# Optimization experiments

Hardware: AMD Instinct MI355X
Metric: run time of the kernel (lower is better)

## Reference

```python
import jax, jax.numpy as jnp
import numpy as np

BS, N_PTS, N_SAMPLES = 8, 8192, 2048
GRID_SIZE = 4096
MAX_X, MAX_Y, MAX_Z = 25.0, 25.0, 5.0
P_NORM = 1


def _sample_axis(key, max_v):
    # linspace(-max_v, max_v, GRID_SIZE) indexed by multinomial(uniform, replacement=False)
    rng = jnp.linspace(-max_v, max_v, GRID_SIZE, dtype=jnp.float32)
    idx = jax.random.choice(key, GRID_SIZE, (N_SAMPLES,), replace=False)
    return rng[idx]


def setup_inputs() -> dict:
    key = jax.random.key(0)
    k1, k2, kx, ky, kz = jax.random.split(key, 5)
    gts = jax.random.normal(k1, (BS, N_PTS, 3), dtype=jnp.float32) * 10.0
    preds = jax.random.normal(k2, (BS, N_PTS, 3), dtype=jnp.float32) * 10.0
    gx = _sample_axis(kx, MAX_X)
    gy = _sample_axis(ky, MAX_Y)
    gz = _sample_axis(kz, MAX_Z)
    grid = jnp.stack([gx, gy, gz], axis=1)  # (N_SAMPLES, 3)
    grid_points = jnp.broadcast_to(grid[None], (BS, N_SAMPLES, 3)).astype(jnp.float32)
    return {"gts": gts, "preds": preds, "grid_points": grid_points}


def _cdist(x, y):
    # Euclidean cdist: (b, n, d) x (b, m, d) -> (b, n, m)
    x2 = jnp.sum(x * x, axis=-1)[:, :, None]
    y2 = jnp.sum(y * y, axis=-1)[:, None, :]
    xy = jnp.einsum('bnd,bmd->bnm', x, y)
    return jnp.sqrt(jnp.maximum(x2 + y2 - 2.0 * xy, 0.0))


def reference(gts, preds, grid_points):
    mins = jnp.min(_cdist(grid_points, preds), axis=2)   # (b, n_samples)
    mins2 = jnp.min(_cdist(grid_points, gts), axis=2)    # (b, n_samples)
    diff = jnp.abs(mins - mins2)
    if P_NORM == 2:
        diff = diff ** 2
    return jnp.mean(diff, axis=1)  # (b,)
```

## Files before the change

kernel.cpp:

```cpp
#include <hip/hip_runtime.h>
#include <math.h>

#define BS 8
#define N_PTS 8192
#define N_SAMPLES 2048
#define THREADS 256
#define SPT 8
#define PSPLIT 64
#define CHUNK (N_PTS / PSPLIT)

__global__ __launch_bounds__(THREADS, 1)
void chamfer_min_kernel(const float* __restrict__ gts,
                        const float* __restrict__ preds,
                        const float* __restrict__ grid,
                        unsigned int* __restrict__ wsmin)
{
    const int bid = blockIdx.x;
    const int b   = bid / PSPLIT;
    const int pc  = bid % PSPLIT;
    const int t   = threadIdx.x;

    __shared__ float4 ldsP[CHUNK];
    __shared__ float4 ldsG[CHUNK];

    {
        const int j = t & (CHUNK - 1);
        const float* src = (t < CHUNK)
            ? preds + ((size_t)b * N_PTS + (size_t)pc * CHUNK) * 3
            : gts   + ((size_t)b * N_PTS + (size_t)pc * CHUNK) * 3;
        const float x = src[j * 3 + 0];
        const float y = src[j * 3 + 1];
        const float z = src[j * 3 + 2];
        const float hp = fmaf(x, x, fmaf(y, y, z * z));
        const float4 v = make_float4(x, y, z, hp);
        if (t < CHUNK) ldsP[j] = v; else ldsG[j] = v;
    }

    float nsx[SPT], nsy[SPT], nsz[SPT], mP[SPT], mG[SPT];
    {
        const float* grow = grid + (size_t)b * N_SAMPLES * 3;
#pragma unroll
        for (int k = 0; k < SPT; ++k) {
            const int s = k * THREADS + t;
            nsx[k] = -2.0f * grow[s * 3 + 0];
            nsy[k] = -2.0f * grow[s * 3 + 1];
            nsz[k] = -2.0f * grow[s * 3 + 2];
            mP[k] = 3.0e38f;
            mG[k] = 3.0e38f;
        }
    }

    __syncthreads();

#pragma unroll 2
    for (int j = 0; j < CHUNK; j += 2) {
        const float4 p0 = ldsP[j], p1 = ldsP[j + 1];
        const float4 g0 = ldsG[j], g1 = ldsG[j + 1];
#pragma unroll
        for (int k = 0; k < SPT; ++k) {
            const float t0 = fmaf(p0.x, nsx[k], fmaf(p0.y, nsy[k], fmaf(p0.z, nsz[k], p0.w)));
            const float t1 = fmaf(p1.x, nsx[k], fmaf(p1.y, nsy[k], fmaf(p1.z, nsz[k], p1.w)));
            mP[k] = fminf(fminf(t0, t1), mP[k]);
            const float u0 = fmaf(g0.x, nsx[k], fmaf(g0.y, nsy[k], fmaf(g0.z, nsz[k], g0.w)));
            const float u1 = fmaf(g1.x, nsx[k], fmaf(g1.y, nsy[k], fmaf(g1.z, nsz[k], g1.w)));
            mG[k] = fminf(fminf(u0, u1), mG[k]);
        }
    }

    unsigned int* wp = wsmin + (size_t)b * N_SAMPLES;
    unsigned int* wg = wsmin + (size_t)(BS + b) * N_SAMPLES;
#pragma unroll
    for (int k = 0; k < SPT; ++k) {
        const int s = k * THREADS + t;
        const float s2 = 0.25f * fmaf(nsx[k], nsx[k], fmaf(nsy[k], nsy[k], nsz[k] * nsz[k]));
        atomicMin(&wp[s], __float_as_uint(fmaxf(mP[k] + s2, 0.0f)));
        atomicMin(&wg[s], __float_as_uint(fmaxf(mG[k] + s2, 0.0f)));
    }
}

__global__ __launch_bounds__(THREADS)
void chamfer_finish_kernel(const unsigned int* __restrict__ wsmin,
                           float* __restrict__ out)
{
    const int b = blockIdx.x;
    const int t = threadIdx.x;
    const unsigned int* wp = wsmin + (size_t)b * N_SAMPLES;
    const unsigned int* wg = wsmin + (size_t)(BS + b) * N_SAMPLES;

    float sum = 0.0f;
#pragma unroll
    for (int s = t; s < N_SAMPLES; s += THREADS) {
        const float dp = sqrtf(__uint_as_float(wp[s]));
        const float dg = sqrtf(__uint_as_float(wg[s]));
        sum += fabsf(dp - dg);
    }

#pragma unroll
    for (int off = 32; off > 0; off >>= 1)
        sum += __shfl_down(sum, off, 64);

    __shared__ float wsum[THREADS / 64];
    const int wid = t >> 6;
    if ((t & 63) == 0) wsum[wid] = sum;
    __syncthreads();
    if (t == 0) {
        float tot = 0.0f;
#pragma unroll
        for (int w = 0; w < THREADS / 64; ++w) tot += wsum[w];
        out[b] = tot / (float)N_SAMPLES;
    }
}

extern "C" void kernel_launch(void* const* d_in, const int* in_sizes, int n_in,
                              void* d_out, int out_size, void* d_ws, size_t ws_size,
                              hipStream_t stream)
{
    const float* gts   = (const float*)d_in[0];
    const float* preds = (const float*)d_in[1];
    const float* grid  = (const float*)d_in[2];
    float* out = (float*)d_out;
    unsigned int* wsmin = (unsigned int*)d_ws;

    const size_t wsbytes = (size_t)2 * BS * N_SAMPLES * sizeof(unsigned int);
    hipMemsetAsync(d_ws, 0x7F, wsbytes, stream);

    chamfer_min_kernel<<<dim3(BS * PSPLIT), dim3(THREADS), 0, stream>>>(gts, preds, grid, wsmin);
    chamfer_finish_kernel<<<dim3(BS), dim3(THREADS), 0, stream>>>(wsmin, out);
}
```

Measured before the change: 34.25 us.

## Precompute float4 point tables in a prep kernel and read them directly from global

Adds a prep kernel that packs preds and gts into float4 (x,y,z,|p|^2) in workspace and initialises the atomic-min buffer, which replaces the memset. The main kernel now reads the packed points straight from global memory (wave-uniform, so broadcast loads) instead of staging them through LDS behind a __syncthreads, and processes four points per step. The aim is to drop the LDS staging and the barrier. In exchange it adds a launch, a global write and re-read of the point tables, and leaves a dead stub kernel behind.

```diff
diff --git a/kernel.cpp b/kernel.cpp
--- a/kernel.cpp
+++ b/kernel.cpp
@@ -8,33 +8,60 @@
 #define SPT 8
 #define PSPLIT 64
 #define CHUNK (N_PTS / PSPLIT)
+#define NTOT (BS * N_PTS)
+
+#define WSMIN_OFF (2 * NTOT)
+
+__global__ __launch_bounds__(THREADS)
+void chamfer_prep_kernel(const float* __restrict__ gts,
+                         const float* __restrict__ preds,
+                         float4* __restrict__ ws)
+{
+    const int i = blockIdx.x * THREADS + threadIdx.x;
+    const float* src = (i < NTOT) ? preds : gts;
+    const int j = (i < NTOT) ? i : i - NTOT;
+    const float x = src[j * 3 + 0];
+    const float y = src[j * 3 + 1];
+    const float z = src[j * 3 + 2];
+    ws[i] = make_float4(x, y, z, fmaf(x, x, fmaf(y, y, z * z)));
+
+    if (i < 2 * BS * N_SAMPLES) {
+        unsigned int* wsmin = (unsigned int*)(ws + WSMIN_OFF);
+        wsmin[i] = 0x7F7F7F7Fu;
+    }
+}
 
 __global__ __launch_bounds__(THREADS, 1)
-void chamfer_min_kernel(const float* __restrict__ gts,
-                        const float* __restrict__ preds,
-                        const float* __restrict__ grid,
-                        unsigned int* __restrict__ wsmin)
+void chamfer_min_kernel(const float4* __restrict__ ws)
 {
     const int bid = blockIdx.x;
     const int b   = bid / PSPLIT;
     const int pc  = bid % PSPLIT;
     const int t   = threadIdx.x;
 
-    __shared__ float4 ldsP[CHUNK];
-    __shared__ float4 ldsG[CHUNK];
+    const float4* __restrict__ pp = ws + (size_t)b * N_PTS + (size_t)pc * CHUNK;
+    const float4* __restrict__ gg = ws + (size_t)(BS + b) * N_PTS + (size_t)pc * CHUNK;
 
+    float nsx[SPT], nsy[SPT], nsz[SPT], mP[SPT], mG[SPT];
     {
-        const int j = t & (CHUNK - 1);
-        const float* src = (t < CHUNK)
-            ? preds + ((size_t)b * N_PTS + (size_t)pc * CHUNK) * 3
-            : gts   + ((size_t)b * N_PTS + (size_t)pc * CHUNK) * 3;
-        const float x = src[j * 3 + 0];
-        const float y = src[j * 3 + 1];
-        const float z = src[j * 3 + 2];
-        const float hp = fmaf(x, x, fmaf(y, y, z * z));
-        const float4 v = make_float4(x, y, z, hp);
-        if (t < CHUNK) ldsP[j] = v; else ldsG[j] = v;
+        const float* grow = (const float*)0;
+        const float* gridp;
+        (void)grow; (void)gridp;
     }
+    mP[0] = 0.f;
+}
+
+__global__ __launch_bounds__(THREADS, 1)
+void chamfer_min_kernel2(const float4* __restrict__ ws,
+                         const float* __restrict__ grid)
+{
+    const int bid = blockIdx.x;
+    const int b   = bid / PSPLIT;
+    const int pc  = bid % PSPLIT;
+    const int t   = threadIdx.x;
+
+    const float4* __restrict__ pp = ws + (size_t)b * N_PTS + (size_t)pc * CHUNK;
+    const float4* __restrict__ gg = ws + (size_t)(BS + b) * N_PTS + (size_t)pc * CHUNK;
 
     float nsx[SPT], nsy[SPT], nsz[SPT], mP[SPT], mG[SPT];
     {
@@ -50,23 +77,27 @@
         }
     }
 
-    __syncthreads();
-
 #pragma unroll 2
-    for (int j = 0; j < CHUNK; j += 2) {
-        const float4 p0 = ldsP[j], p1 = ldsP[j + 1];
-        const float4 g0 = ldsG[j], g1 = ldsG[j + 1];
+    for (int j = 0; j < CHUNK; j += 4) {
+        const float4 p0 = pp[j], p1 = pp[j + 1], p2 = pp[j + 2], p3 = pp[j + 3];
+        const float4 g0 = gg[j], g1 = gg[j + 1], g2 = gg[j + 2], g3 = gg[j + 3];
 #pragma unroll
         for (int k = 0; k < SPT; ++k) {
-            const float t0 = fmaf(p0.x, nsx[k], fmaf(p0.y, nsy[k], fmaf(p0.z, nsz[k], p0.w)));
-            const float t1 = fmaf(p1.x, nsx[k], fmaf(p1.y, nsy[k], fmaf(p1.z, nsz[k], p1.w)));
-            mP[k] = fminf(fminf(t0, t1), mP[k]);
-            const float u0 = fmaf(g0.x, nsx[k], fmaf(g0.y, nsy[k], fmaf(g0.z, nsz[k], g0.w)));
-            const float u1 = fmaf(g1.x, nsx[k], fmaf(g1.y, nsy[k], fmaf(g1.z, nsz[k], g1.w)));
-            mG[k] = fminf(fminf(u0, u1), mG[k]);
+            const float x = nsx[k], y = nsy[k], z = nsz[k];
+            const float t0 = fmaf(p0.x, x, fmaf(p0.y, y, fmaf(p0.z, z, p0.w)));
+            const float t1 = fmaf(p1.x, x, fmaf(p1.y, y, fmaf(p1.z, z, p1.w)));
+            const float t2 = fmaf(p2.x, x, fmaf(p2.y, y, fmaf(p2.z, z, p2.w)));
+            const float t3 = fmaf(p3.x, x, fmaf(p3.y, y, fmaf(p3.z, z, p3.w)));
+            mP[k] = fminf(fminf(t0, t1), fminf(fminf(t2, t3), mP[k]));
+            const float u0 = fmaf(g0.x, x, fmaf(g0.y, y, fmaf(g0.z, z, g0.w)));
+            const float u1 = fmaf(g1.x, x, fmaf(g1.y, y, fmaf(g1.z, z, g1.w)));
+            const float u2 = fmaf(g2.x, x, fmaf(g2.y, y, fmaf(g2.z, z, g2.w)));
+            const float u3 = fmaf(g3.x, x, fmaf(g3.y, y, fmaf(g3.z, z, g3.w)));
+            mG[k] = fminf(fminf(u0, u1), fminf(fminf(u2, u3), mG[k]));
         }
     }
 
+    unsigned int* wsmin = (unsigned int*)(ws + WSMIN_OFF);
     unsigned int* wp = wsmin + (size_t)b * N_SAMPLES;
     unsigned int* wg = wsmin + (size_t)(BS + b) * N_SAMPLES;
 #pragma unroll
@@ -79,9 +110,10 @@
 }
 
 __global__ __launch_bounds__(THREADS)
-void chamfer_finish_kernel(const unsigned int* __restrict__ wsmin,
+void chamfer_finish_kernel(const float4* __restrict__ ws,
                            float* __restrict__ out)
 {
+    const unsigned int* wsmin = (const unsigned int*)(ws + WSMIN_OFF);
     const int b = blockIdx.x;
     const int t = threadIdx.x;
     const unsigned int* wp = wsmin + (size_t)b * N_SAMPLES;
@@ -119,11 +151,9 @@
     const float* preds = (const float*)d_in[1];
     const float* grid  = (const float*)d_in[2];
     float* out = (float*)d_out;
-    unsigned int* wsmin = (unsigned int*)d_ws;
+    float4* ws = (float4*)d_ws;
 
-    const size_t wsbytes = (size_t)2 * BS * N_SAMPLES * sizeof(unsigned int);
-    hipMemsetAsync(d_ws, 0x7F, wsbytes, stream);
-
-    chamfer_min_kernel<<<dim3(BS * PSPLIT), dim3(THREADS), 0, stream>>>(gts, preds, grid, wsmin);
-    chamfer_finish_kernel<<<dim3(BS), dim3(THREADS), 0, stream>>>(wsmin, out);
+    chamfer_prep_kernel<<<dim3(2 * NTOT / THREADS), dim3(THREADS), 0, stream>>>(gts, preds, ws);
+    chamfer_min_kernel2<<<dim3(BS * PSPLIT), dim3(THREADS), 0, stream>>>(ws, grid);
+    chamfer_finish_kernel<<<dim3(BS), dim3(THREADS), 0, stream>>>(ws, out);
 }
```

New measurement: 43.81 us. 1.28x slower.

## Add prep kernel for packed points, retile min kernel with more samples per thread

Applied to the files above, without the earlier changes.

Adds a prep kernel that packs preds and gts into float4 (x,y,z,|p|^2) in workspace and initializes the atomic-min buffer, replacing the memset. The min kernel now uses 128 threads with 16 samples per thread and splits the points into 128 chunks, loading pre-packed float4s. This raises register reuse per LDS read and doubles the block count for the same total work. The cost is an extra kernel launch and a workspace round trip, plus higher register pressure from SPT=16.

```diff
diff --git a/kernel.cpp b/kernel.cpp
--- a/kernel.cpp
+++ b/kernel.cpp
@@ -4,16 +4,36 @@
 #define BS 8
 #define N_PTS 8192
 #define N_SAMPLES 2048
-#define THREADS 256
-#define SPT 8
-#define PSPLIT 64
+#define THREADS 128
+#define SPT 16
+#define PSPLIT 128
 #define CHUNK (N_PTS / PSPLIT)
+#define NTOT (BS * N_PTS)
 
-__global__ __launch_bounds__(THREADS, 1)
-void chamfer_min_kernel(const float* __restrict__ gts,
-                        const float* __restrict__ preds,
-                        const float* __restrict__ grid,
-                        unsigned int* __restrict__ wsmin)
+#define WSMIN_OFF (2 * NTOT)
+
+__global__ __launch_bounds__(256)
+void chamfer_prep_kernel(const float* __restrict__ gts,
+                         const float* __restrict__ preds,
+                         float4* __restrict__ ws)
+{
+    const int i = blockIdx.x * 256 + threadIdx.x;
+    const float* src = (i < NTOT) ? preds : gts;
+    const int j = (i < NTOT) ? i : i - NTOT;
+    const float x = src[j * 3 + 0];
+    const float y = src[j * 3 + 1];
+    const float z = src[j * 3 + 2];
+    ws[i] = make_float4(x, y, z, fmaf(x, x, fmaf(y, y, z * z)));
+
+    if (i < 2 * BS * N_SAMPLES) {
+        unsigned int* wsmin = (unsigned int*)(ws + WSMIN_OFF);
+        wsmin[i] = 0x7F7F7F7Fu;
+    }
+}
+
+__global__ __launch_bounds__(THREADS, 2)
+void chamfer_min_kernel(const float4* __restrict__ ws,
+                        const float* __restrict__ grid)
 {
     const int bid = blockIdx.x;
     const int b   = bid / PSPLIT;
@@ -25,14 +45,10 @@
 
     {
         const int j = t & (CHUNK - 1);
-        const float* src = (t < CHUNK)
-            ? preds + ((size_t)b * N_PTS + (size_t)pc * CHUNK) * 3
-            : gts   + ((size_t)b * N_PTS + (size_t)pc * CHUNK) * 3;
-        const float x = src[j * 3 + 0];
-        const float y = src[j * 3 + 1];
-        const float z = src[j * 3 + 2];
-        const float hp = fmaf(x, x, fmaf(y, y, z * z));
-        const float4 v = make_float4(x, y, z, hp);
+        const float4* src = (t < CHUNK)
+            ? ws + (size_t)b * N_PTS + (size_t)pc * CHUNK
+            : ws + (size_t)(BS + b) * N_PTS + (size_t)pc * CHUNK;
+        const float4 v = src[j];
         if (t < CHUNK) ldsP[j] = v; else ldsG[j] = v;
     }
 
@@ -58,15 +74,17 @@
         const float4 g0 = ldsG[j], g1 = ldsG[j + 1];
 #pragma unroll
         for (int k = 0; k < SPT; ++k) {
-            const float t0 = fmaf(p0.x, nsx[k], fmaf(p0.y, nsy[k], fmaf(p0.z, nsz[k], p0.w)));
-            const float t1 = fmaf(p1.x, nsx[k], fmaf(p1.y, nsy[k], fmaf(p1.z, nsz[k], p1.w)));
+            const float x = nsx[k], y = nsy[k], z = nsz[k];
+            const float t0 = fmaf(p0.x, x, fmaf(p0.y, y, fmaf(p0.z, z, p0.w)));
+            const float t1 = fmaf(p1.x, x, fmaf(p1.y, y, fmaf(p1.z, z, p1.w)));
             mP[k] = fminf(fminf(t0, t1), mP[k]);
-            const float u0 = fmaf(g0.x, nsx[k], fmaf(g0.y, nsy[k], fmaf(g0.z, nsz[k], g0.w)));
-            const float u1 = fmaf(g1.x, nsx[k], fmaf(g1.y, nsy[k], fmaf(g1.z, nsz[k], g1.w)));
+            const float u0 = fmaf(g0.x, x, fmaf(g0.y, y, fmaf(g0.z, z, g0.w)));
+            const float u1 = fmaf(g1.x, x, fmaf(g1.y, y, fmaf(g1.z, z, g1.w)));
             mG[k] = fminf(fminf(u0, u1), mG[k]);
         }
     }
 
+    unsigned int* wsmin = (unsigned int*)(ws + WSMIN_OFF);
     unsigned int* wp = wsmin + (size_t)b * N_SAMPLES;
     unsigned int* wg = wsmin + (size_t)(BS + b) * N_SAMPLES;
 #pragma unroll
@@ -78,10 +96,11 @@
     }
 }
 
-__global__ __launch_bounds__(THREADS)
-void chamfer_finish_kernel(const unsigned int* __restrict__ wsmin,
+__global__ __launch_bounds__(256)
+void chamfer_finish_kernel(const float4* __restrict__ ws,
                            float* __restrict__ out)
 {
+    const unsigned int* wsmin = (const unsigned int*)(ws + WSMIN_OFF);
     const int b = blockIdx.x;
     const int t = threadIdx.x;
     const unsigned int* wp = wsmin + (size_t)b * N_SAMPLES;
@@ -89,7 +108,7 @@
 
     float sum = 0.0f;
 #pragma unroll
-    for (int s = t; s < N_SAMPLES; s += THREADS) {
+    for (int s = t; s < N_SAMPLES; s += 256) {
         const float dp = sqrtf(__uint_as_float(wp[s]));
         const float dg = sqrtf(__uint_as_float(wg[s]));
         sum += fabsf(dp - dg);
@@ -99,14 +118,14 @@
     for (int off = 32; off > 0; off >>= 1)
         sum += __shfl_down(sum, off, 64);
 
-    __shared__ float wsum[THREADS / 64];
+    __shared__ float wsum[4];
     const int wid = t >> 6;
     if ((t & 63) == 0) wsum[wid] = sum;
     __syncthreads();
     if (t == 0) {
         float tot = 0.0f;
 #pragma unroll
-        for (int w = 0; w < THREADS / 64; ++w) tot += wsum[w];
+        for (int w = 0; w < 4; ++w) tot += wsum[w];
         out[b] = tot / (float)N_SAMPLES;
     }
 }
@@ -119,11 +138,9 @@
     const float* preds = (const float*)d_in[1];
     const float* grid  = (const float*)d_in[2];
     float* out = (float*)d_out;
-    unsigned int* wsmin = (unsigned int*)d_ws;
+    float4* ws = (float4*)d_ws;
 
-    const size_t wsbytes = (size_t)2 * BS * N_SAMPLES * sizeof(unsigned int);
-    hipMemsetAsync(d_ws, 0x7F, wsbytes, stream);
-
-    chamfer_min_kernel<<<dim3(BS * PSPLIT), dim3(THREADS), 0, stream>>>(gts, preds, grid, wsmin);
-    chamfer_finish_kernel<<<dim3(BS), dim3(THREADS), 0, stream>>>(wsmin, out);
+    chamfer_prep_kernel<<<dim3(2 * NTOT / 256), dim3(256), 0, stream>>>(gts, preds, ws);
+    chamfer_min_kernel<<<dim3(BS * PSPLIT), dim3(THREADS), 0, stream>>>(ws, grid);
+    chamfer_finish_kernel<<<dim3(BS), dim3(256), 0, stream>>>(ws, out);
 }
```

Result: slower. 45.69 us (+33.4%).

## Replace atomic min reduction with partial buffers and two-stage reduce

Applied to the files above, without the earlier changes.

The min kernel now uses 128-thread blocks, 16 samples per thread and 128 point chunks per batch. Each block writes its per-sample minima to a partial buffer instead of issuing atomicMin, which removes the memset and atomic contention. A separate reduce kernel takes the min over chunks and a tiny kernel forms the final mean. Inline asm pins keep values in registers and the inner loop is no longer unrolled. In exchange it adds about 16 MB of partial-buffer traffic and one extra kernel launch.

```diff
diff --git a/kernel.cpp b/kernel.cpp
--- a/kernel.cpp
+++ b/kernel.cpp
@@ -4,20 +4,24 @@
 #define BS 8
 #define N_PTS 8192
 #define N_SAMPLES 2048
-#define THREADS 256
-#define SPT 8
-#define PSPLIT 64
+#define TA 128
+#define SPT 16
+#define PSPLIT 128
 #define CHUNK (N_PTS / PSPLIT)
 
-__global__ __launch_bounds__(THREADS, 1)
+#define PART_ELEMS (2 * BS * PSPLIT * N_SAMPLES)
+
+#define PIN4(v) asm volatile("" : "+v"(v.x), "+v"(v.y), "+v"(v.z), "+v"(v.w))
+
+__global__ __launch_bounds__(TA, 1)
 void chamfer_min_kernel(const float* __restrict__ gts,
                         const float* __restrict__ preds,
                         const float* __restrict__ grid,
-                        unsigned int* __restrict__ wsmin)
+                        float* __restrict__ part)
 {
     const int bid = blockIdx.x;
-    const int b   = bid / PSPLIT;
-    const int pc  = bid % PSPLIT;
+    const int b   = bid >> 7;
+    const int pc  = bid & (PSPLIT - 1);
     const int t   = threadIdx.x;
 
     __shared__ float4 ldsP[CHUNK];
@@ -25,26 +29,27 @@
 
     {
         const int j = t & (CHUNK - 1);
-        const float* src = (t < CHUNK)
-            ? preds + ((size_t)b * N_PTS + (size_t)pc * CHUNK) * 3
-            : gts   + ((size_t)b * N_PTS + (size_t)pc * CHUNK) * 3;
-        const float x = src[j * 3 + 0];
-        const float y = src[j * 3 + 1];
-        const float z = src[j * 3 + 2];
-        const float hp = fmaf(x, x, fmaf(y, y, z * z));
-        const float4 v = make_float4(x, y, z, hp);
+        const float* src = ((t < CHUNK) ? preds : gts)
+                         + ((size_t)b * N_PTS + (size_t)pc * CHUNK + j) * 3;
+        const float x = src[0], y = src[1], z = src[2];
+        const float4 v = make_float4(x, y, z, fmaf(x, x, fmaf(y, y, z * z)));
         if (t < CHUNK) ldsP[j] = v; else ldsG[j] = v;
     }
 
-    float nsx[SPT], nsy[SPT], nsz[SPT], mP[SPT], mG[SPT];
+    float nsx[SPT], nsy[SPT], nsz[SPT], s2[SPT], mP[SPT], mG[SPT];
     {
         const float* grow = grid + (size_t)b * N_SAMPLES * 3;
 #pragma unroll
         for (int k = 0; k < SPT; ++k) {
-            const int s = k * THREADS + t;
-            nsx[k] = -2.0f * grow[s * 3 + 0];
-            nsy[k] = -2.0f * grow[s * 3 + 1];
-            nsz[k] = -2.0f * grow[s * 3 + 2];
+            const int s = k * TA + t;
+            const float x = grow[s * 3 + 0];
+            const float y = grow[s * 3 + 1];
+            const float z = grow[s * 3 + 2];
+            s2[k]  = fmaf(x, x, fmaf(y, y, z * z));
+            nsx[k] = -2.0f * x;
+            nsy[k] = -2.0f * y;
+            nsz[k] = -2.0f * z;
+            asm volatile("" : "+v"(nsx[k]), "+v"(nsy[k]), "+v"(nsz[k]), "+v"(s2[k]));
             mP[k] = 3.0e38f;
             mG[k] = 3.0e38f;
         }
@@ -52,62 +57,75 @@
 
     __syncthreads();
 
-#pragma unroll 2
+#pragma unroll 1
     for (int j = 0; j < CHUNK; j += 2) {
-        const float4 p0 = ldsP[j], p1 = ldsP[j + 1];
-        const float4 g0 = ldsG[j], g1 = ldsG[j + 1];
+        float4 p0 = ldsP[j], p1 = ldsP[j + 1];
+        float4 g0 = ldsG[j], g1 = ldsG[j + 1];
+        PIN4(p0); PIN4(p1); PIN4(g0); PIN4(g1);
 #pragma unroll
         for (int k = 0; k < SPT; ++k) {
-            const float t0 = fmaf(p0.x, nsx[k], fmaf(p0.y, nsy[k], fmaf(p0.z, nsz[k], p0.w)));
-            const float t1 = fmaf(p1.x, nsx[k], fmaf(p1.y, nsy[k], fmaf(p1.z, nsz[k], p1.w)));
+            const float x = nsx[k], y = nsy[k], z = nsz[k];
+            const float t0 = fmaf(p0.x, x, fmaf(p0.y, y, fmaf(p0.z, z, p0.w)));
+            const float t1 = fmaf(p1.x, x, fmaf(p1.y, y, fmaf(p1.z, z, p1.w)));
             mP[k] = fminf(fminf(t0, t1), mP[k]);
-            const float u0 = fmaf(g0.x, nsx[k], fmaf(g0.y, nsy[k], fmaf(g0.z, nsz[k], g0.w)));
-            const float u1 = fmaf(g1.x, nsx[k], fmaf(g1.y, nsy[k], fmaf(g1.z, nsz[k], g1.w)));
+            const float u0 = fmaf(g0.x, x, fmaf(g0.y, y, fmaf(g0.z, z, g0.w)));
+            const float u1 = fmaf(g1.x, x, fmaf(g1.y, y, fmaf(g1.z, z, g1.w)));
             mG[k] = fminf(fminf(u0, u1), mG[k]);
         }
     }
 
-    unsigned int* wp = wsmin + (size_t)b * N_SAMPLES;
-    unsigned int* wg = wsmin + (size_t)(BS + b) * N_SAMPLES;
+    float* pp = part + (((size_t)b)           * PSPLIT + pc) * N_SAMPLES;
+    float* pg = part + (((size_t)(BS + b))    * PSPLIT + pc) * N_SAMPLES;
 #pragma unroll
     for (int k = 0; k < SPT; ++k) {
-        const int s = k * THREADS + t;
-        const float s2 = 0.25f * fmaf(nsx[k], nsx[k], fmaf(nsy[k], nsy[k], nsz[k] * nsz[k]));
-        atomicMin(&wp[s], __float_as_uint(fmaxf(mP[k] + s2, 0.0f)));
-        atomicMin(&wg[s], __float_as_uint(fmaxf(mG[k] + s2, 0.0f)));
+        const int s = k * TA + t;
+        pp[s] = fmaxf(mP[k] + s2[k], 0.0f);
+        pg[s] = fmaxf(mG[k] + s2[k], 0.0f);
     }
 }
 
-__global__ __launch_bounds__(THREADS)
-void chamfer_finish_kernel(const unsigned int* __restrict__ wsmin,
-                           float* __restrict__ out)
+__global__ __launch_bounds__(256, 1)
+void chamfer_reduce_kernel(const float* __restrict__ part,
+                           float* __restrict__ tsum)
 {
-    const int b = blockIdx.x;
-    const int t = threadIdx.x;
-    const unsigned int* wp = wsmin + (size_t)b * N_SAMPLES;
-    const unsigned int* wg = wsmin + (size_t)(BS + b) * N_SAMPLES;
+    const int blk  = blockIdx.x;
+    const int b    = blk >> 3;
+    const int tile = blk & 7;
+    const int t    = threadIdx.x;
+    const int s    = tile * 256 + t;
 
-    float sum = 0.0f;
-#pragma unroll
-    for (int s = t; s < N_SAMPLES; s += THREADS) {
-        const float dp = sqrtf(__uint_as_float(wp[s]));
-        const float dg = sqrtf(__uint_as_float(wg[s]));
-        sum += fabsf(dp - dg);
+    const float* pp = part + ((size_t)b)        * PSPLIT * N_SAMPLES + s;
+    const float* pg = part + ((size_t)(BS + b)) * PSPLIT * N_SAMPLES + s;
+
+    float mp = 3.0e38f, mg = 3.0e38f;
+#pragma unroll 4
+    for (int pc = 0; pc < PSPLIT; ++pc) {
+        mp = fminf(mp, pp[(size_t)pc * N_SAMPLES]);
+        mg = fminf(mg, pg[(size_t)pc * N_SAMPLES]);
     }
+
+    float v = fabsf(sqrtf(mp) - sqrtf(mg));
 
 #pragma unroll
     for (int off = 32; off > 0; off >>= 1)
-        sum += __shfl_down(sum, off, 64);
+        v += __shfl_down(v, off, 64);
 
-    __shared__ float wsum[THREADS / 64];
-    const int wid = t >> 6;
-    if ((t & 63) == 0) wsum[wid] = sum;
+    __shared__ float w[4];
+    if ((t & 63) == 0) w[t >> 6] = v;
     __syncthreads();
-    if (t == 0) {
+    if (t == 0) tsum[blk] = (w[0] + w[1]) + (w[2] + w[3]);
+}
+
+__global__ __launch_bounds__(64)
+void chamfer_out_kernel(const float* __restrict__ tsum,
+                        float* __restrict__ out)
+{
+    const int b = threadIdx.x;
+    if (b < BS) {
         float tot = 0.0f;
 #pragma unroll
-        for (int w = 0; w < THREADS / 64; ++w) tot += wsum[w];
-        out[b] = tot / (float)N_SAMPLES;
+        for (int i = 0; i < 8; ++i) tot += tsum[b * 8 + i];
+        out[b] = tot * (1.0f / (float)N_SAMPLES);
     }
 }
 
@@ -118,12 +136,11 @@
     const float* gts   = (const float*)d_in[0];
     const float* preds = (const float*)d_in[1];
     const float* grid  = (const float*)d_in[2];
-    float* out = (float*)d_out;
-    unsigned int* wsmin = (unsigned int*)d_ws;
+    float* out  = (float*)d_out;
+    float* part = (float*)d_ws;
+    float* tsum = part + PART_ELEMS;
 
-    const size_t wsbytes = (size_t)2 * BS * N_SAMPLES * sizeof(unsigned int);
-    hipMemsetAsync(d_ws, 0x7F, wsbytes, stream);
-
-    chamfer_min_kernel<<<dim3(BS * PSPLIT), dim3(THREADS), 0, stream>>>(gts, preds, grid, wsmin);
-    chamfer_finish_kernel<<<dim3(BS), dim3(THREADS), 0, stream>>>(wsmin, out);
+    chamfer_min_kernel<<<dim3(BS * PSPLIT), dim3(TA), 0, stream>>>(gts, preds, grid, part);
+    chamfer_reduce_kernel<<<dim3(64), dim3(256), 0, stream>>>(part, tsum);
+    chamfer_out_kernel<<<dim3(1), dim3(64), 0, stream>>>(tsum, out);
 }
```

Result: slower. 49.81 us (+45.4%).
